# Kernel tuning notes

Hardware: AMD Instinct MI355X
Metric: run time of the kernel (lower is better)

The kernel has to match this reference:

```python
import jax, jax.numpy as jnp
import numpy as np

B, S, E = 2, 2048, 1024          # batch, seq, emb_size
H, D = 16, 64                     # heads, head_dim
NE, K = 8, 2                      # num_experts, top_k


def setup_inputs() -> dict:
    key = jax.random.key(0)
    ks = jax.random.split(key, 12)
    w = lambda k, shape: jax.random.normal(k, shape, jnp.float32) * 0.02
    return {
        "x": jax.random.normal(ks[0], (B, S, E), jnp.float32),
        "q_w": w(ks[1], (E, E)), "q_b": jnp.zeros((E,), jnp.float32),
        "k_w": w(ks[2], (E, E)), "k_b": jnp.zeros((E,), jnp.float32),
        "v_w": w(ks[3], (E, E)), "v_b": jnp.zeros((E,), jnp.float32),
        "gate_w": w(ks[4], (NE, E)), "gate_b": jnp.zeros((NE,), jnp.float32),
        "expert_w": w(ks[5], (NE, E, E)), "expert_b": jnp.zeros((NE, E), jnp.float32),
        "ffn_w": w(ks[6], (E, E)), "ffn_b": jnp.zeros((E,), jnp.float32),
    }


def _rope_cos_sin(seq_len, dim):
    inv_freq = 1.0 / (10000.0 ** (jnp.arange(0, dim, 2, dtype=jnp.float32) / dim))
    freqs = jnp.outer(jnp.arange(seq_len, dtype=jnp.float32), inv_freq)  # [S, D/2]
    emb = jnp.concatenate([freqs, freqs], axis=-1)                        # [S, D]
    return jnp.cos(emb), jnp.sin(emb)


def _rotate_half(x):
    x1, x2 = jnp.split(x, 2, axis=-1)
    return jnp.concatenate([-x2, x1], axis=-1)


def reference(x, q_w, q_b, k_w, k_b, v_w, v_b, gate_w, gate_b, expert_w, expert_b, ffn_w, ffn_b):
    b, s, _ = x.shape
    q = (x @ q_w.T + q_b).reshape(b, s, H, D)
    k = (x @ k_w.T + k_b).reshape(b, s, H, D)
    v = (x @ v_w.T + v_b).reshape(b, s, H, D)

    cos, sin = _rope_cos_sin(s, D)          # [S, D]
    cos = cos[None, :, None, :]
    sin = sin[None, :, None, :]
    q = q * cos + _rotate_half(q) * sin
    k = k * cos + _rotate_half(k) * sin

    # full (memory-efficient-style) attention, scale 1/sqrt(D)
    scores = jnp.einsum('bqhd,bkhd->bhqk', q, k) / jnp.sqrt(jnp.float32(D))
    attn = jax.nn.softmax(scores, axis=-1)
    attn_out = jnp.einsum('bhqk,bkhd->bqhd', attn, v).reshape(b, s, E)

    # MoE: dense-compute all experts, gather top-k, weighted combine
    gates = jax.nn.softmax(attn_out @ gate_w.T + gate_b, axis=-1)        # [B,S,NE]
    top_gates, top_idx = jax.lax.top_k(gates, K)                          # [B,S,K]
    # Linear per expert: y = x W^T + b,  expert_w: [NE, out, in]
    expert_outputs = jnp.einsum('bsi,noi->bsno', attn_out, expert_w) + expert_b  # [B,S,NE,E]
    sel = jnp.take_along_axis(expert_outputs, top_idx[..., None], axis=2)        # [B,S,K,E]
    moe_out = jnp.einsum('bsk,bskh->bsh', top_gates, sel)                        # [B,S,E]

    # dropout is identity at inference; ffn + residual
    return moe_out @ ffn_w.T + ffn_b + x
```

## Files before the change

kernel.cpp:

```cpp
#include <hip/hip_runtime.h>
#include <hip/hip_bf16.h>

#define B_ 2
#define S_ 2048
#define E_ 1024
#define H_ 16
#define D_ 64
#define NE_ 8
#define TOKENS (B_*S_)
#define QSCALE 0.18033688011112043f

typedef __attribute__((ext_vector_type(8))) short bf16x8;
typedef __attribute__((ext_vector_type(4))) float f32x4;
typedef unsigned short u16;
typedef unsigned int u32;

#if __has_builtin(__builtin_amdgcn_exp2f)
#define EXP2(x) __builtin_amdgcn_exp2f(x)
#else
#define EXP2(x) exp2f(x)
#endif

__device__ __forceinline__ u16 f2bf(float f) {
    u32 u = __float_as_uint(f);
    u32 r = u + 0x7fffu + ((u >> 16) & 1u);
    return (u16)(r >> 16);
}
__device__ __forceinline__ float bf2f(u16 h) {
    return __uint_as_float(((u32)h) << 16);
}
__device__ __forceinline__ void gl2lds16(const void* g, void* l) {
    __builtin_amdgcn_global_load_lds(
        (__attribute__((address_space(1))) void*)(g),
        (__attribute__((address_space(3))) void*)(l), 16, 0, 0);
}
#define MFMA16(a,b,c) __builtin_amdgcn_mfma_f32_16x16x32_bf16(a,b,c,0,0,0)

__global__ void cvt_all_k(
    const float* __restrict__ x,  const float* __restrict__ qw,
    const float* __restrict__ kw, const float* __restrict__ vw,
    const float* __restrict__ fw, const float* __restrict__ ew,
    u16* __restrict__ xh,  u16* __restrict__ qwh, u16* __restrict__ kwh,
    u16* __restrict__ vwh, u16* __restrict__ fwh, u16* __restrict__ ewh,
    float2* __restrict__ tab)
{
    const int blk = blockIdx.x;
    if (blk >= 16384) {
        const int idx = (blk - 16384) * 256 + threadIdx.x;
        const int s = idx >> 5, d1 = idx & 31;
        const float inv = exp2f(-(float)d1 * 0.41524101186091903f);
        float sn, cs;
        sincosf((float)s * inv, &sn, &cs);
        tab[idx] = make_float2(cs, sn);
        return;
    }
    const float* s; u16* d; int off;
    if (blk < 4096)      { s = x;  d = xh;  off = blk; }
    else if (blk < 5120) { s = qw; d = qwh; off = blk - 4096; }
    else if (blk < 6144) { s = kw; d = kwh; off = blk - 5120; }
    else if (blk < 7168) { s = vw; d = vwh; off = blk - 6144; }
    else if (blk < 8192) { s = fw; d = fwh; off = blk - 7168; }
    else                 { s = ew; d = ewh; off = blk - 8192; }
    const size_t i = (size_t)off * 256 + threadIdx.x;
    const float4 v = *(const float4*)(s + i * 4);
    ushort4 H = {f2bf(v.x), f2bf(v.y), f2bf(v.z), f2bf(v.w)};
    *(ushort4*)(d + i * 4) = H;
}

__global__ __launch_bounds__(256,2) void gemm_qkv(
    const u16* __restrict__ Ah,
    const u16* __restrict__ qwh, const u16* __restrict__ kwh,
    const u16* __restrict__ vwh,
    const float* __restrict__ q_b, const float* __restrict__ k_b,
    const float* __restrict__ v_b,
    const float2* __restrict__ tab,
    u16* __restrict__ Qhb, u16* __restrict__ Khb, u16* __restrict__ Vtb)
{
    __shared__ __align__(16) u16 sA[128*32], sB[128*32];
    const int z = blockIdx.z;
    const u16* Bh = (z == 0) ? qwh : (z == 1) ? kwh : vwh;
    const float* bias = (z == 0) ? q_b : (z == 1) ? k_b : v_b;
    const int t = threadIdx.x;
    const int m0 = blockIdx.y * 128, n0 = blockIdx.x * 128;
    const int lane = t & 63, w = t >> 6;
    const int wm = w >> 1, wn = w & 1;
    const int lr = lane & 15, qd = lane >> 4;
    f32x4 acc[4][4] = {};
    const size_t gA = (size_t)(m0 + (t >> 2)) * E_ + (t & 3) * 8;
    const size_t gB = (size_t)(n0 + (t >> 2)) * E_ + (t & 3) * 8;
    for (int k0 = 0; k0 < E_; k0 += 32) {
        #pragma unroll
        for (int is = 0; is < 2; is++) {
            const int ldo = (is * 256 + (t & 192)) * 16;
            const size_t ro = (size_t)is * 64 * E_;
            gl2lds16(Ah + gA + ro + k0, (char*)sA + ldo);
            gl2lds16(Bh + gB + ro + k0, (char*)sB + ldo);
        }
        __syncthreads();
        bf16x8 af[4], bfr[4];
        #pragma unroll
        for (int i = 0; i < 4; i++) {
            af[i]  = *(const bf16x8*)&sA[(wm*64 + i*16 + lr)*32 + qd*8];
            bfr[i] = *(const bf16x8*)&sB[(wn*64 + i*16 + lr)*32 + qd*8];
        }
        #pragma unroll
        for (int i = 0; i < 4; i++)
            #pragma unroll
            for (int j = 0; j < 4; j++)
                acc[i][j] = MFMA16(af[i], bfr[j], acc[i][j]);
        __syncthreads();
    }
    const int head = (n0 + wn * 64) >> 6;
    if (z < 2) {
        u16* Oh = (z == 0) ? Qhb : Khb;
        const float osc = (z == 0) ? QSCALE : 1.0f;
        #pragma unroll
        for (int j = 0; j < 2; j++) {
            const int d1 = j * 16 + lr;
            const float b1 = bias[head * 64 + d1];
            const float b2 = bias[head * 64 + d1 + 32];
            #pragma unroll
            for (int i = 0; i < 4; i++) {
                #pragma unroll
                for (int r = 0; r < 4; r++) {
                    const int tok = m0 + wm*64 + i*16 + qd*4 + r;
                    const int bb = tok >> 11, ss = tok & (S_ - 1);
                    const float2 t2 = tab[ss * 32 + d1];
                    const float q1 = acc[i][j][r]   + b1;
                    const float q2 = acc[i][j+2][r] + b2;
                    const size_t o = (((size_t)bb * H_ + head) * S_ + ss) * 64 + d1;
                    Oh[o]    = f2bf((q1 * t2.x - q2 * t2.y) * osc);
                    Oh[o+32] = f2bf((q2 * t2.x + q1 * t2.y) * osc);
                }
            }
        }
    } else {
        #pragma unroll
        for (int j = 0; j < 4; j++) {
            const int d = j * 16 + lr;
            const float bv = bias[head * 64 + d];
            #pragma unroll
            for (int i = 0; i < 4; i++)
                #pragma unroll
                for (int r = 0; r < 4; r++) {
                    const int tok = m0 + wm*64 + i*16 + qd*4 + r;
                    const int bb = tok >> 11, ss = tok & (S_ - 1);
                    Vtb[(((size_t)bb * H_ + head) * 64 + d) * S_ + ss] = f2bf(acc[i][j][r] + bv);
                }
        }
    }
}

__global__ __launch_bounds__(256,4) void attn_kernel(
    const u16* __restrict__ Q, const u16* __restrict__ K,
    const u16* __restrict__ Vt,
    float* __restrict__ Opart, float* __restrict__ lpart)
{
    __shared__ __align__(16) u16 sK[64*64];
    __shared__ __align__(16) u16 sV[64*64];
    __shared__ __align__(16) u16 sP[4][2][16*40];
    const int t = threadIdx.x, lane = t & 63, w = t >> 6;
    const int lr = lane & 15, qd = lane >> 4;
    const int q0 = blockIdx.x * 128;
    const int h = blockIdx.y;
    const int b = blockIdx.z & 1, sc = blockIdx.z >> 1;
    const size_t bhS = ((size_t)b * H_ + h) * S_;
    const size_t bhD = ((size_t)b * H_ + h) * 64;
    bf16x8 qf[2][2];
    #pragma unroll
    for (int p = 0; p < 2; p++) {
        const size_t qa = (bhS + q0 + p*64 + w*16 + lr) * 64 + qd * 8;
        qf[p][0] = *(const bf16x8*)&Q[qa];
        qf[p][1] = *(const bf16x8*)&Q[qa + 32];
    }
    bf16x8 vOnes;
    #pragma unroll
    for (int i = 0; i < 8; i++) vOnes[i] = (short)0x3F80;
    f32x4 O[2][4] = {};
    f32x4 Ol[2] = {};
    const int jbeg = sc * 1024, jend = jbeg + 1024;
    for (int j0 = jbeg; j0 < jend; j0 += 64) {
        #pragma unroll
        for (int it = 0; it < 2; it++) {
            const int CH = (it*4 + w)*4 + qd;
            const int sbs = CH >> 3;
            const int doff = ((CH >> 2) & 1)*32 + (CH & 3)*8;
            gl2lds16(&K [(bhS + j0 + sbs*16 + lr)*64 + doff],
                     (char*)sK + (it*4 + w)*1024);
            gl2lds16(&Vt[(bhD + sbs*16 + lr)*S_ + j0 + doff],
                     (char*)sV + (it*4 + w)*1024);
        }
        __syncthreads();
        f32x4 Sv[2][4];
        #pragma unroll
        for (int sb = 0; sb < 4; sb++) {
            bf16x8 k0 = *(const bf16x8*)&sK[(sb*8 + qd)*128 + lr*8];
            bf16x8 k1 = *(const bf16x8*)&sK[(sb*8 + 4 + qd)*128 + lr*8];
            f32x4 a0 = {}, a1 = {};
            a0 = MFMA16(k0, qf[0][0], a0);
            a0 = MFMA16(k1, qf[0][1], a0);
            a1 = MFMA16(k0, qf[1][0], a1);
            a1 = MFMA16(k1, qf[1][1], a1);
            Sv[0][sb] = a0;
            Sv[1][sb] = a1;
        }
        #pragma unroll
        for (int p = 0; p < 2; p++) {
            #pragma unroll
            for (int sb = 0; sb < 4; sb++) {
                const float pv0 = EXP2(Sv[p][sb][0]);
                const float pv1 = EXP2(Sv[p][sb][1]);
                const float pv2 = EXP2(Sv[p][sb][2]);
                const float pv3 = EXP2(Sv[p][sb][3]);
                uint2 pk;
                pk.x = __builtin_amdgcn_perm(__float_as_uint(pv1),
                                             __float_as_uint(pv0), 0x07060302u);
                pk.y = __builtin_amdgcn_perm(__float_as_uint(pv3),
                                             __float_as_uint(pv2), 0x07060302u);
                *(uint2*)&sP[w][p][lr*40 + sb*16 + qd*4] = pk;
            }
        }
        {
            bf16x8 vv[8];
            #pragma unroll
            for (int ds = 0; ds < 4; ds++) {
                vv[2*ds]   = *(const bf16x8*)&sV[(ds*8 + qd)*128 + lr*8];
                vv[2*ds+1] = *(const bf16x8*)&sV[(ds*8 + 4 + qd)*128 + lr*8];
            }
            #pragma unroll
            for (int p = 0; p < 2; p++) {
                bf16x8 p0 = *(const bf16x8*)&sP[w][p][lr*40 + qd*8];
                bf16x8 p1 = *(const bf16x8*)&sP[w][p][lr*40 + 32 + qd*8];
                #pragma unroll
                for (int ds = 0; ds < 4; ds++) {
                    O[p][ds] = MFMA16(p0, vv[2*ds],   O[p][ds]);
                    O[p][ds] = MFMA16(p1, vv[2*ds+1], O[p][ds]);
                }
                Ol[p] = MFMA16(p0, vOnes, Ol[p]);
                Ol[p] = MFMA16(p1, vOnes, Ol[p]);
            }
        }
        __syncthreads();
    }
    float* Op = Opart + (size_t)sc * TOKENS * E_;
    float* lp = lpart + (size_t)sc * TOKENS * H_;
    if (lr == 0) {
        #pragma unroll
        for (int p = 0; p < 2; p++)
            #pragma unroll
            for (int r = 0; r < 4; r++)
                lp[(size_t)(b*S_ + q0 + p*64 + w*16 + qd*4 + r) * H_ + h] = Ol[p][r];
    }
    #pragma unroll
    for (int p = 0; p < 2; p++) {
        const int qb = q0 + p*64 + w*16 + qd*4;
        #pragma unroll
        for (int ds = 0; ds < 4; ds++)
            #pragma unroll
            for (int r = 0; r < 4; r++)
                Op[(size_t)(b*S_ + qb + r) * E_ + h*64 + ds*16 + lr] = O[p][ds][r];
    }
}

__global__ __launch_bounds__(256) void combine_gate(
    const float* __restrict__ Opart, const float* __restrict__ lpart,
    const float* __restrict__ gate_w, const float* __restrict__ gate_b,
    u16* __restrict__ attn_bf, float* __restrict__ gval, int* __restrict__ eidx)
{
    __shared__ float red[4][NE_];
    __shared__ float lg8[NE_];
    const int tok = blockIdx.x;
    const int t = threadIdx.x;
    const int d4 = t * 4;
    const int h = d4 >> 6;
    const float l = lpart[(size_t)tok*H_ + h] + lpart[(size_t)(TOKENS + tok)*H_ + h];
    const float inv = 1.f / l;
    const float4 o1 = *(const float4*)&Opart[(size_t)tok*E_ + d4];
    const float4 o2 = *(const float4*)&Opart[(size_t)(TOKENS + tok)*E_ + d4];
    float v[4] = {(o1.x+o2.x)*inv, (o1.y+o2.y)*inv, (o1.z+o2.z)*inv, (o1.w+o2.w)*inv};
    ushort4 H4 = {f2bf(v[0]), f2bf(v[1]), f2bf(v[2]), f2bf(v[3])};
    *(ushort4*)&attn_bf[(size_t)tok*E_ + d4] = H4;
    float pe[NE_];
    #pragma unroll
    for (int e = 0; e < NE_; e++) {
        const float4 g = *(const float4*)&gate_w[e*E_ + d4];
        pe[e] = v[0]*g.x + v[1]*g.y + v[2]*g.z + v[3]*g.w;
    }
    #pragma unroll
    for (int e = 0; e < NE_; e++) {
        #pragma unroll
        for (int off = 32; off >= 1; off >>= 1)
            pe[e] += __shfl_xor(pe[e], off, 64);
    }
    const int w = t >> 6;
    if ((t & 63) == 0) {
        #pragma unroll
        for (int e = 0; e < NE_; e++) red[w][e] = pe[e];
    }
    __syncthreads();
    if (t < NE_)
        lg8[t] = red[0][t] + red[1][t] + red[2][t] + red[3][t] + gate_b[t];
    __syncthreads();
    if (t == 0) {
        float lg[NE_];
        #pragma unroll
        for (int e = 0; e < NE_; e++) lg[e] = lg8[e];
        float m = lg[0];
        #pragma unroll
        for (int e = 1; e < NE_; e++) m = fmaxf(m, lg[e]);
        float ex[NE_], ssum = 0.f;
        #pragma unroll
        for (int e = 0; e < NE_; e++) { ex[e] = __expf(lg[e]-m); ssum += ex[e]; }
        const float invs = 1.f / ssum;
        int i0 = 0;
        #pragma unroll
        for (int e = 1; e < NE_; e++) if (lg[e] > lg[i0]) i0 = e;
        int i1 = (i0 == 0) ? 1 : 0;
        #pragma unroll
        for (int e = 0; e < NE_; e++) if (e != i0 && lg[e] > lg[i1]) i1 = e;
        eidx[tok*2]     = i0;
        gval[tok*2]     = ex[i0]*invs;
        eidx[tok*2 + 1] = i1;
        gval[tok*2 + 1] = ex[i1]*invs;
    }
}

__global__ __launch_bounds__(256) void build_lists_kernel(
    const int* __restrict__ eidx, int* __restrict__ list, int* __restrict__ counts)
{
    __shared__ int lcnt[NE_], lbase[NE_];
    const int t = threadIdx.x;
    if (t < NE_) lcnt[t] = 0;
    __syncthreads();
    const int ent = blockIdx.x * 512 + t * 2;
    const int e0 = eidx[ent], e1 = eidx[ent + 1];
    const int p0 = atomicAdd(&lcnt[e0], 1);
    const int p1 = atomicAdd(&lcnt[e1], 1);
    __syncthreads();
    if (t < NE_) lbase[t] = atomicAdd(&counts[t], lcnt[t]);
    __syncthreads();
    list[e0 * TOKENS + lbase[e0] + p0] = ent;
    list[e1 * TOKENS + lbase[e1] + p1] = ent + 1;
}

__global__ __launch_bounds__(256,2) void gemm_expert(
    const u16* __restrict__ Abf, const u16* __restrict__ ewh,
    const float* __restrict__ eb, const int* __restrict__ list,
    const int* __restrict__ counts, const float* __restrict__ gval,
    u16* __restrict__ sel)
{
    const int e = blockIdx.z;
    const int cnt = counts[e];
    const int m0 = blockIdx.y * 128;
    if (m0 >= cnt) return;
    __shared__ __align__(16) u16 sA[128*32], sB[128*32];
    __shared__ int sEnt[128];
    const int t = threadIdx.x;
    if (t < 128) sEnt[t] = (m0 + t < cnt) ? list[e * TOKENS + m0 + t] : -1;
    __syncthreads();
    const int n0 = blockIdx.x * 128;
    const int lane = t & 63, w = t >> 6;
    const int wm = w >> 1, wn = w & 1;
    const int lr = lane & 15, qd = lane >> 4;
    const int e0 = sEnt[t >> 2], e1 = sEnt[64 + (t >> 2)];
    const u16* ga0 = Abf + (size_t)(e0 < 0 ? 0 : (e0 >> 1)) * E_ + (t & 3) * 8;
    const u16* ga1 = Abf + (size_t)(e1 < 0 ? 0 : (e1 >> 1)) * E_ + (t & 3) * 8;
    const u16* gb0 = ewh + (size_t)e * E_ * E_ + (size_t)(n0 + (t >> 2)) * E_ + (t & 3) * 8;
    const u16* gb1 = gb0 + 64 * E_;
    f32x4 acc[4][4] = {};
    for (int k0 = 0; k0 < E_; k0 += 32) {
        {
            const int l0 = (t & 192) * 16;
            const int l1 = (256 + (t & 192)) * 16;
            gl2lds16(ga0 + k0, (char*)sA + l0);
            gl2lds16(ga1 + k0, (char*)sA + l1);
            gl2lds16(gb0 + k0, (char*)sB + l0);
            gl2lds16(gb1 + k0, (char*)sB + l1);
        }
        __syncthreads();
        bf16x8 af[4], bfr[4];
        #pragma unroll
        for (int i = 0; i < 4; i++) {
            af[i]  = *(const bf16x8*)&sA[(wm*64 + i*16 + lr)*32 + qd*8];
            bfr[i] = *(const bf16x8*)&sB[(wn*64 + i*16 + lr)*32 + qd*8];
        }
        #pragma unroll
        for (int i = 0; i < 4; i++)
            #pragma unroll
            for (int j = 0; j < 4; j++)
                acc[i][j] = MFMA16(af[i], bfr[j], acc[i][j]);
        __syncthreads();
    }
    #pragma unroll
    for (int i = 0; i < 4; i++)
        #pragma unroll
        for (int r = 0; r < 4; r++) {
            const int local = wm*64 + i*16 + qd*4 + r;
            const int ent = sEnt[local];
            if (ent < 0) continue;
            const float g = gval[ent];
            #pragma unroll
            for (int j = 0; j < 4; j++) {
                const int col = n0 + wn*64 + j*16 + lr;
                sel[(size_t)ent * E_ + col] = f2bf((acc[i][j][r] + eb[e * E_ + col]) * g);
            }
        }
}

__global__ void combine_kernel(const u16* __restrict__ sel, u16* __restrict__ moe)
{
    const int g = blockIdx.x * 256 + threadIdx.x;
    const int tok = g >> 8;
    const int c = (g & 255) * 4;
    const u16* a = sel + (size_t)tok * 2048 + c;
    float o[4];
    #pragma unroll
    for (int j = 0; j < 4; j++) o[j] = bf2f(a[j]) + bf2f(a[1024 + j]);
    ushort4 R = {f2bf(o[0]), f2bf(o[1]), f2bf(o[2]), f2bf(o[3])};
    *(ushort4*)(moe + (size_t)tok * E_ + c) = R;
}

__global__ __launch_bounds__(256,2) void gemm_ffn(
    const u16* __restrict__ Ah, const u16* __restrict__ Bh,
    const float* __restrict__ bias, const float* __restrict__ res,
    float* __restrict__ C)
{
    __shared__ __align__(16) u16 sA[128*32], sB[128*32];
    const int t = threadIdx.x;
    const int m0 = blockIdx.y * 128, n0 = blockIdx.x * 128;
    const int lane = t & 63, w = t >> 6;
    const int wm = w >> 1, wn = w & 1;
    const int lr = lane & 15, qd = lane >> 4;
    f32x4 acc[4][4] = {};
    const size_t gA = (size_t)(m0 + (t >> 2)) * E_ + (t & 3) * 8;
    const size_t gB = (size_t)(n0 + (t >> 2)) * E_ + (t & 3) * 8;
    for (int k0 = 0; k0 < E_; k0 += 32) {
        #pragma unroll
        for (int is = 0; is < 2; is++) {
            const int ldo = (is * 256 + (t & 192)) * 16;
            const size_t ro = (size_t)is * 64 * E_;
            gl2lds16(Ah + gA + ro + k0, (char*)sA + ldo);
            gl2lds16(Bh + gB + ro + k0, (char*)sB + ldo);
        }
        __syncthreads();
        bf16x8 af[4], bfr[4];
        #pragma unroll
        for (int i = 0; i < 4; i++) {
            af[i]  = *(const bf16x8*)&sA[(wm*64 + i*16 + lr)*32 + qd*8];
            bfr[i] = *(const bf16x8*)&sB[(wn*64 + i*16 + lr)*32 + qd*8];
        }
        #pragma unroll
        for (int i = 0; i < 4; i++)
            #pragma unroll
            for (int j = 0; j < 4; j++)
                acc[i][j] = MFMA16(af[i], bfr[j], acc[i][j]);
        __syncthreads();
    }
    #pragma unroll
    for (int i = 0; i < 4; i++)
        #pragma unroll
        for (int r = 0; r < 4; r++) {
            const int tok = m0 + wm*64 + i*16 + qd*4 + r;
            #pragma unroll
            for (int j = 0; j < 4; j++) {
                const int col = n0 + wn*64 + j*16 + lr;
                C[(size_t)tok * E_ + col] = acc[i][j][r] + bias[col] + res[(size_t)tok * E_ + col];
            }
        }
}

extern "C" void kernel_launch(void* const* d_in, const int* in_sizes, int n_in,
                              void* d_out, int out_size, void* d_ws, size_t ws_size,
                              hipStream_t stream) {
    const float* x      = (const float*)d_in[0];
    const float* q_w    = (const float*)d_in[1];
    const float* q_b    = (const float*)d_in[2];
    const float* k_w    = (const float*)d_in[3];
    const float* k_b    = (const float*)d_in[4];
    const float* v_w    = (const float*)d_in[5];
    const float* v_b    = (const float*)d_in[6];
    const float* gate_w = (const float*)d_in[7];
    const float* gate_b = (const float*)d_in[8];
    const float* ew     = (const float*)d_in[9];
    const float* eb     = (const float*)d_in[10];
    const float* ffn_w  = (const float*)d_in[11];
    const float* ffn_b  = (const float*)d_in[12];
    float* out = (float*)d_out;

    char* p = (char*)d_ws;
    auto alloc = [&](size_t bytes) { char* r = p; p += (bytes + 255) & ~(size_t)255; return r; };
    u16* xh   = (u16*)alloc((size_t)TOKENS*E_*2);
    u16* qwh  = (u16*)alloc((size_t)E_*E_*2);
    u16* kwh  = (u16*)alloc((size_t)E_*E_*2);
    u16* vwh  = (u16*)alloc((size_t)E_*E_*2);
    u16* fwh  = (u16*)alloc((size_t)E_*E_*2);
    u16* ewh  = (u16*)alloc((size_t)NE_*E_*E_*2);
    u16* Qhb  = (u16*)alloc((size_t)TOKENS*E_*2);
    u16* Khb  = (u16*)alloc((size_t)TOKENS*E_*2);
    u16* Vtb  = (u16*)alloc((size_t)TOKENS*E_*2);
    u16* abf  = (u16*)alloc((size_t)TOKENS*E_*2);
    float* Opart = (float*)alloc((size_t)2*TOKENS*E_*4);
    float* lpart = (float*)alloc((size_t)2*TOKENS*H_*4);
    u16* selb = (u16*)alloc((size_t)2*TOKENS*E_*2);
    u16* moeb = (u16*)alloc((size_t)TOKENS*E_*2);
    float2* rtab = (float2*)alloc((size_t)S_*32*8);
    float* gvl = (float*)alloc((size_t)2*TOKENS*4);
    int*   eix = (int*)alloc((size_t)2*TOKENS*4);
    int*   lst = (int*)alloc((size_t)NE_*TOKENS*4);
    int*   cnt = (int*)alloc(256);

    hipMemsetAsync(cnt, 0, 256, stream);

    cvt_all_k<<<16640, 256, 0, stream>>>(x, q_w, k_w, v_w, ffn_w, ew,
                                         xh, qwh, kwh, vwh, fwh, ewh, rtab);

    gemm_qkv<<<dim3(8,32,3), 256, 0, stream>>>(xh, qwh, kwh, vwh,
                                               q_b, k_b, v_b, rtab,
                                               Qhb, Khb, Vtb);

    attn_kernel<<<dim3(16,16,4), 256, 0, stream>>>(Qhb, Khb, Vtb, Opart, lpart);

    combine_gate<<<TOKENS, 256, 0, stream>>>(Opart, lpart, gate_w, gate_b,
                                             abf, gvl, eix);
    build_lists_kernel<<<TOKENS/256, 256, 0, stream>>>(eix, lst, cnt);
    gemm_expert<<<dim3(8,32,8), 256, 0, stream>>>(abf, ewh, eb, lst, cnt, gvl, selb);
    combine_kernel<<<4096, 256, 0, stream>>>(selb, moeb);
    gemm_ffn<<<dim3(8,32), 256, 0, stream>>>(moeb, fwh, ffn_b, x, out);
}
```

Measured before the change: 291.9 us.

## Drop attention split-K, double-buffer K/V loads, fuse normalization into attention

The attention kernel now walks the full key range per block instead of splitting it into two halves, so the fp32 partial outputs and the separate combine pass are gone. The kernel normalizes and writes bf16 output directly. K/V tiles are double-buffered in LDS with prefetch of the next tile, plus MFMA priority hints and a block-index swizzle. Gating becomes a one-wave-per-token kernel that reads the bf16 attention output. In exchange the grid is half as large, with lower occupancy per block (launch bounds 2), and gate logits are now computed from bf16-rounded activations.

```diff
diff --git a/kernel.cpp b/kernel.cpp
--- a/kernel.cpp
+++ b/kernel.cpp
@@ -151,19 +151,20 @@
     }
 }
 
-__global__ __launch_bounds__(256,4) void attn_kernel(
+__global__ __launch_bounds__(256,2) void attn_kernel(
     const u16* __restrict__ Q, const u16* __restrict__ K,
-    const u16* __restrict__ Vt,
-    float* __restrict__ Opart, float* __restrict__ lpart)
-{
-    __shared__ __align__(16) u16 sK[64*64];
-    __shared__ __align__(16) u16 sV[64*64];
+    const u16* __restrict__ Vt, u16* __restrict__ attn_bf)
+{
+    __shared__ __align__(16) u16 sK[2][64*64];
+    __shared__ __align__(16) u16 sV[2][64*64];
     __shared__ __align__(16) u16 sP[4][2][16*40];
     const int t = threadIdx.x, lane = t & 63, w = t >> 6;
     const int lr = lane & 15, qd = lane >> 4;
-    const int q0 = blockIdx.x * 128;
-    const int h = blockIdx.y;
-    const int b = blockIdx.z & 1, sc = blockIdx.z >> 1;
+    const int lin = blockIdx.x + (blockIdx.y << 4) + (blockIdx.z << 8);
+    const int wg  = ((lin & 7) << 6) + (lin >> 3);
+    const int q0 = (wg & 15) << 7;
+    const int h  = (wg >> 4) & 15;
+    const int b  = wg >> 8;
     const size_t bhS = ((size_t)b * H_ + h) * S_;
     const size_t bhD = ((size_t)b * H_ + h) * 64;
     bf16x8 qf[2][2];
@@ -178,24 +179,31 @@
     for (int i = 0; i < 8; i++) vOnes[i] = (short)0x3F80;
     f32x4 O[2][4] = {};
     f32x4 Ol[2] = {};
-    const int jbeg = sc * 1024, jend = jbeg + 1024;
-    for (int j0 = jbeg; j0 < jend; j0 += 64) {
-        #pragma unroll
-        for (int it = 0; it < 2; it++) {
-            const int CH = (it*4 + w)*4 + qd;
-            const int sbs = CH >> 3;
-            const int doff = ((CH >> 2) & 1)*32 + (CH & 3)*8;
-            gl2lds16(&K [(bhS + j0 + sbs*16 + lr)*64 + doff],
-                     (char*)sK + (it*4 + w)*1024);
-            gl2lds16(&Vt[(bhD + sbs*16 + lr)*S_ + j0 + doff],
-                     (char*)sV + (it*4 + w)*1024);
-        }
-        __syncthreads();
+
+    const int CH0 = w*4 + qd, CH1 = (4 + w)*4 + qd;
+    const int sbs0 = CH0 >> 3, doff0 = ((CH0 >> 2) & 1)*32 + (CH0 & 3)*8;
+    const int sbs1 = CH1 >> 3, doff1 = ((CH1 >> 2) & 1)*32 + (CH1 & 3)*8;
+    auto stage = [&](int bp, int j0) {
+        gl2lds16(&K [(bhS + j0 + sbs0*16 + lr)*64 + doff0], (char*)sK[bp] + w*1024);
+        gl2lds16(&Vt[(bhD + sbs0*16 + lr)*S_ + j0 + doff0], (char*)sV[bp] + w*1024);
+        gl2lds16(&K [(bhS + j0 + sbs1*16 + lr)*64 + doff1], (char*)sK[bp] + (4+w)*1024);
+        gl2lds16(&Vt[(bhD + sbs1*16 + lr)*S_ + j0 + doff1], (char*)sV[bp] + (4+w)*1024);
+    };
+
+    stage(0, 0);
+    for (int jt = 0; jt < 32; ++jt) {
+        const int cur = jt & 1;
+        asm volatile("s_waitcnt vmcnt(0) lgkmcnt(0)" ::: "memory");
+        __builtin_amdgcn_sched_barrier(0);
+        __builtin_amdgcn_s_barrier();
+        __builtin_amdgcn_sched_barrier(0);
+        if (jt + 1 < 32) stage(cur ^ 1, (jt + 1) * 64);
         f32x4 Sv[2][4];
+        __builtin_amdgcn_s_setprio(1);
         #pragma unroll
         for (int sb = 0; sb < 4; sb++) {
-            bf16x8 k0 = *(const bf16x8*)&sK[(sb*8 + qd)*128 + lr*8];
-            bf16x8 k1 = *(const bf16x8*)&sK[(sb*8 + 4 + qd)*128 + lr*8];
+            bf16x8 k0 = *(const bf16x8*)&sK[cur][(sb*8 + qd)*128 + lr*8];
+            bf16x8 k1 = *(const bf16x8*)&sK[cur][(sb*8 + 4 + qd)*128 + lr*8];
             f32x4 a0 = {}, a1 = {};
             a0 = MFMA16(k0, qf[0][0], a0);
             a0 = MFMA16(k1, qf[0][1], a0);
@@ -204,6 +212,7 @@
             Sv[0][sb] = a0;
             Sv[1][sb] = a1;
         }
+        __builtin_amdgcn_s_setprio(0);
         #pragma unroll
         for (int p = 0; p < 2; p++) {
             #pragma unroll
@@ -224,9 +233,10 @@
             bf16x8 vv[8];
             #pragma unroll
             for (int ds = 0; ds < 4; ds++) {
-                vv[2*ds]   = *(const bf16x8*)&sV[(ds*8 + qd)*128 + lr*8];
-                vv[2*ds+1] = *(const bf16x8*)&sV[(ds*8 + 4 + qd)*128 + lr*8];
+                vv[2*ds]   = *(const bf16x8*)&sV[cur][(ds*8 + qd)*128 + lr*8];
+                vv[2*ds+1] = *(const bf16x8*)&sV[cur][(ds*8 + 4 + qd)*128 + lr*8];
             }
+            __builtin_amdgcn_s_setprio(1);
             #pragma unroll
             for (int p = 0; p < 2; p++) {
                 bf16x8 p0 = *(const bf16x8*)&sP[w][p][lr*40 + qd*8];
@@ -239,52 +249,42 @@
                 Ol[p] = MFMA16(p0, vOnes, Ol[p]);
                 Ol[p] = MFMA16(p1, vOnes, Ol[p]);
             }
-        }
-        __syncthreads();
-    }
-    float* Op = Opart + (size_t)sc * TOKENS * E_;
-    float* lp = lpart + (size_t)sc * TOKENS * H_;
-    if (lr == 0) {
-        #pragma unroll
-        for (int p = 0; p < 2; p++)
-            #pragma unroll
-            for (int r = 0; r < 4; r++)
-                lp[(size_t)(b*S_ + q0 + p*64 + w*16 + qd*4 + r) * H_ + h] = Ol[p][r];
+            __builtin_amdgcn_s_setprio(0);
+        }
     }
     #pragma unroll
     for (int p = 0; p < 2; p++) {
-        const int qb = q0 + p*64 + w*16 + qd*4;
-        #pragma unroll
-        for (int ds = 0; ds < 4; ds++)
-            #pragma unroll
-            for (int r = 0; r < 4; r++)
-                Op[(size_t)(b*S_ + qb + r) * E_ + h*64 + ds*16 + lr] = O[p][ds][r];
-    }
-}
-
-__global__ __launch_bounds__(256) void combine_gate(
-    const float* __restrict__ Opart, const float* __restrict__ lpart,
-    const float* __restrict__ gate_w, const float* __restrict__ gate_b,
-    u16* __restrict__ attn_bf, float* __restrict__ gval, int* __restrict__ eidx)
-{
-    __shared__ float red[4][NE_];
-    __shared__ float lg8[NE_];
-    const int tok = blockIdx.x;
-    const int t = threadIdx.x;
-    const int d4 = t * 4;
-    const int h = d4 >> 6;
-    const float l = lpart[(size_t)tok*H_ + h] + lpart[(size_t)(TOKENS + tok)*H_ + h];
-    const float inv = 1.f / l;
-    const float4 o1 = *(const float4*)&Opart[(size_t)tok*E_ + d4];
-    const float4 o2 = *(const float4*)&Opart[(size_t)(TOKENS + tok)*E_ + d4];
-    float v[4] = {(o1.x+o2.x)*inv, (o1.y+o2.y)*inv, (o1.z+o2.z)*inv, (o1.w+o2.w)*inv};
-    ushort4 H4 = {f2bf(v[0]), f2bf(v[1]), f2bf(v[2]), f2bf(v[3])};
-    *(ushort4*)&attn_bf[(size_t)tok*E_ + d4] = H4;
-    float pe[NE_];
-    #pragma unroll
-    for (int e = 0; e < NE_; e++) {
-        const float4 g = *(const float4*)&gate_w[e*E_ + d4];
-        pe[e] = v[0]*g.x + v[1]*g.y + v[2]*g.z + v[3]*g.w;
+        #pragma unroll
+        for (int r = 0; r < 4; r++) {
+            const float inv = 1.0f / Ol[p][r];
+            const int q = q0 + p*64 + w*16 + qd*4 + r;
+            u16* orow = attn_bf + ((size_t)b * S_ + q) * E_ + h * 64 + lr;
+            #pragma unroll
+            for (int ds = 0; ds < 4; ds++)
+                orow[ds*16] = f2bf(O[p][ds][r] * inv);
+        }
+    }
+}
+
+__global__ __launch_bounds__(256) void gate_topk(
+    const u16* __restrict__ A, const float* __restrict__ gate_w,
+    const float* __restrict__ gate_b,
+    float* __restrict__ gval, int* __restrict__ eidx)
+{
+    const int t = threadIdx.x, lane = t & 63, w = t >> 6;
+    const int tok = blockIdx.x * 4 + w;
+    const u16* a = A + (size_t)tok * E_ + lane * 16;
+    float pe[NE_] = {};
+    #pragma unroll
+    for (int c = 0; c < 4; c++) {
+        const ushort4 a4 = *(const ushort4*)&a[c * 4];
+        const float v0 = bf2f(a4.x), v1 = bf2f(a4.y);
+        const float v2 = bf2f(a4.z), v3 = bf2f(a4.w);
+        #pragma unroll
+        for (int e = 0; e < NE_; e++) {
+            const float4 g = *(const float4*)&gate_w[e * E_ + lane * 16 + c * 4];
+            pe[e] += v0*g.x + v1*g.y + v2*g.z + v3*g.w;
+        }
     }
     #pragma unroll
     for (int e = 0; e < NE_; e++) {
@@ -292,19 +292,10 @@
         for (int off = 32; off >= 1; off >>= 1)
             pe[e] += __shfl_xor(pe[e], off, 64);
     }
-    const int w = t >> 6;
-    if ((t & 63) == 0) {
-        #pragma unroll
-        for (int e = 0; e < NE_; e++) red[w][e] = pe[e];
-    }
-    __syncthreads();
-    if (t < NE_)
-        lg8[t] = red[0][t] + red[1][t] + red[2][t] + red[3][t] + gate_b[t];
-    __syncthreads();
-    if (t == 0) {
+    if (lane == 0) {
         float lg[NE_];
         #pragma unroll
-        for (int e = 0; e < NE_; e++) lg[e] = lg8[e];
+        for (int e = 0; e < NE_; e++) lg[e] = pe[e] + gate_b[e];
         float m = lg[0];
         #pragma unroll
         for (int e = 1; e < NE_; e++) m = fmaxf(m, lg[e]);
@@ -499,8 +490,6 @@
     u16* Khb  = (u16*)alloc((size_t)TOKENS*E_*2);
     u16* Vtb  = (u16*)alloc((size_t)TOKENS*E_*2);
     u16* abf  = (u16*)alloc((size_t)TOKENS*E_*2);
-    float* Opart = (float*)alloc((size_t)2*TOKENS*E_*4);
-    float* lpart = (float*)alloc((size_t)2*TOKENS*H_*4);
     u16* selb = (u16*)alloc((size_t)2*TOKENS*E_*2);
     u16* moeb = (u16*)alloc((size_t)TOKENS*E_*2);
     float2* rtab = (float2*)alloc((size_t)S_*32*8);
@@ -518,10 +507,9 @@
                                                q_b, k_b, v_b, rtab,
                                                Qhb, Khb, Vtb);
 
-    attn_kernel<<<dim3(16,16,4), 256, 0, stream>>>(Qhb, Khb, Vtb, Opart, lpart);
-
-    combine_gate<<<TOKENS, 256, 0, stream>>>(Opart, lpart, gate_w, gate_b,
-                                             abf, gvl, eix);
+    attn_kernel<<<dim3(16,16,2), 256, 0, stream>>>(Qhb, Khb, Vtb, abf);
+
+    gate_topk<<<TOKENS/4, 256, 0, stream>>>(abf, gate_w, gate_b, gvl, eix);
     build_lists_kernel<<<TOKENS/256, 256, 0, stream>>>(eix, lst, cnt);
     gemm_expert<<<dim3(8,32,8), 256, 0, stream>>>(abf, ewh, eb, lst, cnt, gvl, selb);
     combine_kernel<<<4096, 256, 0, stream>>>(selb, moeb);
```

Result: no change. 294.6 us (+0.9%).

## Double-buffer K/V tiles in attention and remap workgroups for XCD locality

Applied to the files above, without the earlier changes.

Attention now double-buffers the K and V shared-memory tiles, so the next 64-key tile is prefetched while the current one is consumed, and one barrier per iteration replaces two. The workgroup index is remapped so consecutive blocks on the same XCD share head/batch data in L2. It also shrinks the P scratch buffer by reusing one buffer per wave, and raises wave priority around the MFMA sections. This costs extra LDS, which may lower occupancy, and the single buffer for P adds ordering constraints within each wave.

```diff
diff --git a/kernel.cpp b/kernel.cpp
--- a/kernel.cpp
+++ b/kernel.cpp
@@ -156,14 +156,17 @@
     const u16* __restrict__ Vt,
     float* __restrict__ Opart, float* __restrict__ lpart)
 {
-    __shared__ __align__(16) u16 sK[64*64];
-    __shared__ __align__(16) u16 sV[64*64];
-    __shared__ __align__(16) u16 sP[4][2][16*40];
+    __shared__ __align__(16) u16 sK[2][64*64];
+    __shared__ __align__(16) u16 sV[2][64*64];
+    __shared__ __align__(16) u16 sP[4][672];
     const int t = threadIdx.x, lane = t & 63, w = t >> 6;
     const int lr = lane & 15, qd = lane >> 4;
-    const int q0 = blockIdx.x * 128;
-    const int h = blockIdx.y;
-    const int b = blockIdx.z & 1, sc = blockIdx.z >> 1;
+    const int lin = blockIdx.x + (blockIdx.y << 4) + (blockIdx.z << 8);
+    const int wg  = ((lin & 7) << 7) + (lin >> 3);
+    const int q0 = (wg & 15) << 7;
+    const int h  = (wg >> 4) & 15;
+    const int zc = wg >> 8;
+    const int b = zc & 1, sc = zc >> 1;
     const size_t bhS = ((size_t)b * H_ + h) * S_;
     const size_t bhD = ((size_t)b * H_ + h) * 64;
     bf16x8 qf[2][2];
@@ -178,24 +181,32 @@
     for (int i = 0; i < 8; i++) vOnes[i] = (short)0x3F80;
     f32x4 O[2][4] = {};
     f32x4 Ol[2] = {};
-    const int jbeg = sc * 1024, jend = jbeg + 1024;
-    for (int j0 = jbeg; j0 < jend; j0 += 64) {
-        #pragma unroll
-        for (int it = 0; it < 2; it++) {
-            const int CH = (it*4 + w)*4 + qd;
-            const int sbs = CH >> 3;
-            const int doff = ((CH >> 2) & 1)*32 + (CH & 3)*8;
-            gl2lds16(&K [(bhS + j0 + sbs*16 + lr)*64 + doff],
-                     (char*)sK + (it*4 + w)*1024);
-            gl2lds16(&Vt[(bhD + sbs*16 + lr)*S_ + j0 + doff],
-                     (char*)sV + (it*4 + w)*1024);
-        }
-        __syncthreads();
+
+    const int CH0 = w*4 + qd, CH1 = (4 + w)*4 + qd;
+    const int sbs0 = CH0 >> 3, doff0 = ((CH0 >> 2) & 1)*32 + (CH0 & 3)*8;
+    const int sbs1 = CH1 >> 3, doff1 = ((CH1 >> 2) & 1)*32 + (CH1 & 3)*8;
+    auto stage = [&](int bp, int j0) {
+        gl2lds16(&K [(bhS + j0 + sbs0*16 + lr)*64 + doff0], (char*)sK[bp] + w*1024);
+        gl2lds16(&Vt[(bhD + sbs0*16 + lr)*S_ + j0 + doff0], (char*)sV[bp] + w*1024);
+        gl2lds16(&K [(bhS + j0 + sbs1*16 + lr)*64 + doff1], (char*)sK[bp] + (4+w)*1024);
+        gl2lds16(&Vt[(bhD + sbs1*16 + lr)*S_ + j0 + doff1], (char*)sV[bp] + (4+w)*1024);
+    };
+
+    const int jbeg = sc * 1024;
+    stage(0, jbeg);
+    for (int jt = 0; jt < 16; ++jt) {
+        const int cur = jt & 1;
+        asm volatile("s_waitcnt vmcnt(0) lgkmcnt(0)" ::: "memory");
+        __builtin_amdgcn_sched_barrier(0);
+        __builtin_amdgcn_s_barrier();
+        __builtin_amdgcn_sched_barrier(0);
+        if (jt + 1 < 16) stage(cur ^ 1, jbeg + (jt + 1) * 64);
         f32x4 Sv[2][4];
+        __builtin_amdgcn_s_setprio(1);
         #pragma unroll
         for (int sb = 0; sb < 4; sb++) {
-            bf16x8 k0 = *(const bf16x8*)&sK[(sb*8 + qd)*128 + lr*8];
-            bf16x8 k1 = *(const bf16x8*)&sK[(sb*8 + 4 + qd)*128 + lr*8];
+            bf16x8 k0 = *(const bf16x8*)&sK[cur][(sb*8 + qd)*128 + lr*8];
+            bf16x8 k1 = *(const bf16x8*)&sK[cur][(sb*8 + 4 + qd)*128 + lr*8];
             f32x4 a0 = {}, a1 = {};
             a0 = MFMA16(k0, qf[0][0], a0);
             a0 = MFMA16(k1, qf[0][1], a0);
@@ -204,6 +215,8 @@
             Sv[0][sb] = a0;
             Sv[1][sb] = a1;
         }
+        __builtin_amdgcn_s_setprio(0);
+        uint2 pk[2][4];
         #pragma unroll
         for (int p = 0; p < 2; p++) {
             #pragma unroll
@@ -212,35 +225,35 @@
                 const float pv1 = EXP2(Sv[p][sb][1]);
                 const float pv2 = EXP2(Sv[p][sb][2]);
                 const float pv3 = EXP2(Sv[p][sb][3]);
-                uint2 pk;
-                pk.x = __builtin_amdgcn_perm(__float_as_uint(pv1),
-                                             __float_as_uint(pv0), 0x07060302u);
-                pk.y = __builtin_amdgcn_perm(__float_as_uint(pv3),
-                                             __float_as_uint(pv2), 0x07060302u);
-                *(uint2*)&sP[w][p][lr*40 + sb*16 + qd*4] = pk;
+                pk[p][sb].x = __builtin_amdgcn_perm(__float_as_uint(pv1),
+                                                    __float_as_uint(pv0), 0x07060302u);
+                pk[p][sb].y = __builtin_amdgcn_perm(__float_as_uint(pv3),
+                                                    __float_as_uint(pv2), 0x07060302u);
             }
         }
-        {
-            bf16x8 vv[8];
+        bf16x8 vv[8];
+        #pragma unroll
+        for (int ds = 0; ds < 4; ds++) {
+            vv[2*ds]   = *(const bf16x8*)&sV[cur][(ds*8 + qd)*128 + lr*8];
+            vv[2*ds+1] = *(const bf16x8*)&sV[cur][(ds*8 + 4 + qd)*128 + lr*8];
+        }
+        #pragma unroll
+        for (int p = 0; p < 2; p++) {
+            #pragma unroll
+            for (int sb = 0; sb < 4; sb++)
+                *(uint2*)&sP[w][lr*40 + sb*16 + qd*4] = pk[p][sb];
+            bf16x8 p0 = *(const bf16x8*)&sP[w][lr*40 + qd*8];
+            bf16x8 p1 = *(const bf16x8*)&sP[w][lr*40 + 32 + qd*8];
+            __builtin_amdgcn_s_setprio(1);
             #pragma unroll
             for (int ds = 0; ds < 4; ds++) {
-                vv[2*ds]   = *(const bf16x8*)&sV[(ds*8 + qd)*128 + lr*8];
-                vv[2*ds+1] = *(const bf16x8*)&sV[(ds*8 + 4 + qd)*128 + lr*8];
+                O[p][ds] = MFMA16(p0, vv[2*ds],   O[p][ds]);
+                O[p][ds] = MFMA16(p1, vv[2*ds+1], O[p][ds]);
             }
-            #pragma unroll
-            for (int p = 0; p < 2; p++) {
-                bf16x8 p0 = *(const bf16x8*)&sP[w][p][lr*40 + qd*8];
-                bf16x8 p1 = *(const bf16x8*)&sP[w][p][lr*40 + 32 + qd*8];
-                #pragma unroll
-                for (int ds = 0; ds < 4; ds++) {
-                    O[p][ds] = MFMA16(p0, vv[2*ds],   O[p][ds]);
-                    O[p][ds] = MFMA16(p1, vv[2*ds+1], O[p][ds]);
-                }
-                Ol[p] = MFMA16(p0, vOnes, Ol[p]);
-                Ol[p] = MFMA16(p1, vOnes, Ol[p]);
-            }
-        }
-        __syncthreads();
+            Ol[p] = MFMA16(p0, vOnes, Ol[p]);
+            Ol[p] = MFMA16(p1, vOnes, Ol[p]);
+            __builtin_amdgcn_s_setprio(0);
+        }
     }
     float* Op = Opart + (size_t)sc * TOKENS * E_;
     float* lp = lpart + (size_t)sc * TOKENS * H_;
```

Result: no change. 289.7 us (-0.8%).
